# Performance work log

Hardware: AMD Instinct MI355X
Metric: run time of the kernel (lower is better)

Reference implementation:

```python
import jax, jax.numpy as jnp
import numpy as np

B, H, D, E = 64, 8, 64, 512          # batch, heads, head_dim, embed_dim
NB, BS = 32, 128                     # blocks per sequence, block size
L = NB * BS                          # max kv length (4096)
POS = 2048                           # decode position in cache


def setup_inputs() -> dict:
    key = jax.random.key(0)
    ks = jax.random.split(key, 12)
    s = E ** -0.5
    return {
        "hidden_states": jax.random.normal(ks[0], (B, 1, E), jnp.float32),
        "q_w": jax.random.normal(ks[1], (E, E), jnp.float32) * s,
        "q_b": jnp.zeros((E,), jnp.float32),
        "k_w": jax.random.normal(ks[2], (E, E), jnp.float32) * s,
        "k_b": jnp.zeros((E,), jnp.float32),
        "v_w": jax.random.normal(ks[3], (E, E), jnp.float32) * s,
        "v_b": jnp.zeros((E,), jnp.float32),
        "o_w": jax.random.normal(ks[4], (E, E), jnp.float32) * s,
        "o_b": jnp.zeros((E,), jnp.float32),
        "kcache": jax.random.normal(ks[5], (B, H, NB, BS, D), jnp.float32),
        "vcache": jax.random.normal(ks[6], (B, H, NB, BS, D), jnp.float32),
        "attention_mask": jnp.zeros((B, 1, 1, L), jnp.float32),  # additive mask
        "cache_position": POS,
        "block_tables": jax.random.randint(ks[7], (B, NB), 0, NB, jnp.int32),
    }


def reference(hidden_states, q_w, q_b, k_w, k_b, v_w, v_b, o_w, o_b,
              kcache, vcache, attention_mask, cache_position, block_tables):
    scaling = D ** -0.5
    # projections for the single decode token; q is pre-scaled (op gets scale=1.0)
    q = (hidden_states[:, 0] @ q_w.T + q_b).reshape(B, H, D) * scaling
    k_new = (hidden_states[:, 0] @ k_w.T + k_b).reshape(B, H, D)
    v_new = (hidden_states[:, 0] @ v_w.T + v_b).reshape(B, H, D)

    # gather physical blocks per sequence via block table -> [B, NB, H, BS, D]
    bidx = jnp.arange(B)[:, None]
    k_g = kcache[bidx, :, block_tables].transpose(0, 2, 1, 3, 4).reshape(B, H, L, D)
    v_g = vcache[bidx, :, block_tables].transpose(0, 2, 1, 3, 4).reshape(B, H, L, D)

    # write current token's k/v at cache_position (paged cache update)
    k_g = k_g.at[:, :, cache_position, :].set(k_new)
    v_g = v_g.at[:, :, cache_position, :].set(v_new)

    # add-softmax attention: scores = qk + mask
    scores = jnp.einsum('bhd,bhld->bhl', q, k_g) + attention_mask[:, :, 0, :]
    attn = jax.nn.softmax(scores, axis=-1)
    ctx = jnp.einsum('bhl,bhld->bhd', attn, v_g).reshape(B, 1, E)
    return ctx @ o_w.T + o_b
```

## Files before the change

kernel.cpp:

```cpp
#include <hip/hip_runtime.h>
#include <math.h>

#define BB 64
#define HH 8
#define Dh 64
#define EE 512
#define NBLK 32
#define BSZ 128
#define LL 4096
#define BG 4
#define RC 128

typedef float f4 __attribute__((ext_vector_type(4)));

__global__ __launch_bounds__(512) void qkv_proj(
    const float* __restrict__ hidden,
    const float* __restrict__ q_w, const float* __restrict__ q_b,
    const float* __restrict__ k_w, const float* __restrict__ k_b,
    const float* __restrict__ v_w, const float* __restrict__ v_b,
    float* __restrict__ ws)
{
    const int bg = blockIdx.x, proj = blockIdx.y, chunk = blockIdx.z;
    const int tid = threadIdx.x;
    const int r  = tid & (RC - 1);
    const int l4 = tid >> 7;

    __shared__ float sh[BG][EE];
    __shared__ float sp[4][BG][RC];

    for (int i = tid; i < BG * EE; i += 512)
        sh[i >> 9][i & (EE - 1)] = hidden[(bg * BG + (i >> 9)) * EE + (i & (EE - 1))];
    __syncthreads();

    const float* w; const float* bias; float* out; float scale;
    if (proj == 0)      { w = q_w; bias = q_b; out = ws;             scale = 0.125f; }
    else if (proj == 1) { w = k_w; bias = k_b; out = ws + BB * EE;   scale = 1.0f; }
    else                { w = v_w; bias = v_b; out = ws + 2*BB*EE;   scale = 1.0f; }

    const int e = chunk * RC + r;
    const float4* wr = (const float4*)(w + (size_t)e * EE + l4 * 128);
    float acc[BG] = {0.f, 0.f, 0.f, 0.f};
    #pragma unroll 8
    for (int i = 0; i < 32; ++i) {
        const float4 a = wr[i];
        #pragma unroll
        for (int b = 0; b < BG; ++b) {
            const float4 x = ((const float4*)sh[b])[l4 * 32 + i];
            acc[b] += a.x*x.x + a.y*x.y + a.z*x.z + a.w*x.w;
        }
    }
    #pragma unroll
    for (int b = 0; b < BG; ++b) sp[l4][b][r] = acc[b];
    __syncthreads();

    const int b2 = tid >> 7, r2 = tid & (RC - 1);
    const int e2 = chunk * RC + r2;
    const float v = sp[0][b2][r2] + sp[1][b2][r2] + sp[2][b2][r2] + sp[3][b2][r2];
    out[(bg * BG + b2) * EE + e2] = (v + bias[e2]) * scale;
}

__global__ __launch_bounds__(512) void attn(
    const float* __restrict__ ws,
    const float* __restrict__ kcache, const float* __restrict__ vcache,
    const float* __restrict__ mask,
    const int* __restrict__ cpos_p,
    const int* __restrict__ btab,
    float* __restrict__ ctx)
{
    const int bh = blockIdx.x;
    const int b  = bh >> 3;
    const int tid = threadIdx.x;
    const int grp = tid >> 4;
    const int l16 = tid & 15;

    __shared__ float  s_q[Dh];
    __shared__ int    s_bt[NBLK];
    __shared__ float  s_m[32];
    __shared__ float  s_s[32];
    __shared__ float4 s_acc[32][16];

    const float* qv   = ws;
    const float* knew = ws + BB * EE;
    const float* vnew = ws + 2 * BB * EE;

    if (tid < Dh)   s_q[tid]  = qv[(size_t)bh * Dh + tid];
    if (tid < NBLK) s_bt[tid] = btab[b * NBLK + tid];
    const int cpos = *cpos_p;
    __syncthreads();

    const float4 q4 = ((const float4*)s_q)[l16];
    const size_t base = (size_t)bh * NBLK * BSZ * Dh;
    const f4* knew4 = (const f4*)(knew + (size_t)bh * Dh);
    const f4* vnew4 = (const f4*)(vnew + (size_t)bh * Dh);
    const float* mrow = mask + (size_t)b * LL;

    float m = -3.4e38f, s = 0.f;
    float4 acc = make_float4(0.f, 0.f, 0.f, 0.f);

    #pragma unroll 2
    for (int c = 0; c < NBLK; ++c) {
        const size_t pb = base + (size_t)s_bt[c] * (BSZ * Dh);
        #pragma unroll
        for (int s4 = 0; s4 < 4; ++s4) {
            const int rl  = s4 * 32 + grp;
            const int row = c * BSZ + rl;
            const f4* kr = (const f4*)(kcache + pb + (size_t)rl * Dh);
            const f4* vr = (const f4*)(vcache + pb + (size_t)rl * Dh);
            if (row == cpos) { kr = knew4; vr = vnew4; }
            const f4 kv = __builtin_nontemporal_load(kr + l16);
            const f4 vv = __builtin_nontemporal_load(vr + l16);

            float p = q4.x*kv.x + q4.y*kv.y + q4.z*kv.z + q4.w*kv.w;
            p += __shfl_xor(p, 1); p += __shfl_xor(p, 2);
            p += __shfl_xor(p, 4); p += __shfl_xor(p, 8);
            p += mrow[row];

            const float mn = fmaxf(m, p);
            const float cr = __expf(m - mn);
            const float wt = __expf(p - mn);
            s = s * cr + wt;
            acc.x = acc.x * cr + wt * vv.x;
            acc.y = acc.y * cr + wt * vv.y;
            acc.z = acc.z * cr + wt * vv.z;
            acc.w = acc.w * cr + wt * vv.w;
            m = mn;
        }
    }

    if (l16 == 0) { s_m[grp] = m; s_s[grp] = s; }
    s_acc[grp][l16] = acc;
    __syncthreads();

    if (tid < 32) {
        const float mg = s_m[tid];
        float M = mg;
        #pragma unroll
        for (int o = 1; o < 32; o <<= 1) M = fmaxf(M, __shfl_xor(M, o));
        const float c = __expf(mg - M);
        float st = s_s[tid] * c;
        #pragma unroll
        for (int o = 1; o < 32; o <<= 1) st += __shfl_xor(st, o);
        s_m[tid] = c;
        if (tid == 0) s_s[0] = 1.0f / st;
    }
    __syncthreads();

    if (tid < 16) {
        const float inv = s_s[0];
        float4 t = make_float4(0.f, 0.f, 0.f, 0.f);
        #pragma unroll
        for (int g = 0; g < 32; ++g) {
            const float c = s_m[g];
            const float4 u = s_acc[g][tid];
            t.x += c * u.x; t.y += c * u.y; t.z += c * u.z; t.w += c * u.w;
        }
        t.x *= inv; t.y *= inv; t.z *= inv; t.w *= inv;
        ((float4*)(ctx + (size_t)bh * Dh))[tid] = t;
    }
}

__global__ __launch_bounds__(512) void out_proj(
    const float* __restrict__ ctx,
    const float* __restrict__ o_w, const float* __restrict__ o_b,
    float* __restrict__ out)
{
    const int bg = blockIdx.x, chunk = blockIdx.y;
    const int tid = threadIdx.x;
    const int r  = tid & (RC - 1);
    const int l4 = tid >> 7;

    __shared__ float sh[BG][EE];
    __shared__ float sp[4][BG][RC];

    for (int i = tid; i < BG * EE; i += 512)
        sh[i >> 9][i & (EE - 1)] = ctx[(bg * BG + (i >> 9)) * EE + (i & (EE - 1))];
    __syncthreads();

    const int e = chunk * RC + r;
    const float4* wr = (const float4*)(o_w + (size_t)e * EE + l4 * 128);
    float acc[BG] = {0.f, 0.f, 0.f, 0.f};
    #pragma unroll 8
    for (int i = 0; i < 32; ++i) {
        const float4 a = wr[i];
        #pragma unroll
        for (int b = 0; b < BG; ++b) {
            const float4 x = ((const float4*)sh[b])[l4 * 32 + i];
            acc[b] += a.x*x.x + a.y*x.y + a.z*x.z + a.w*x.w;
        }
    }
    #pragma unroll
    for (int b = 0; b < BG; ++b) sp[l4][b][r] = acc[b];
    __syncthreads();

    const int b2 = tid >> 7, r2 = tid & (RC - 1);
    const int e2 = chunk * RC + r2;
    const float v = sp[0][b2][r2] + sp[1][b2][r2] + sp[2][b2][r2] + sp[3][b2][r2];
    out[(bg * BG + b2) * EE + e2] = v + o_b[e2];
}

extern "C" void kernel_launch(void* const* d_in, const int* in_sizes, int n_in,
                              void* d_out, int out_size, void* d_ws, size_t ws_size,
                              hipStream_t stream)
{
    const float* hidden = (const float*)d_in[0];
    const float* q_w = (const float*)d_in[1];
    const float* q_b = (const float*)d_in[2];
    const float* k_w = (const float*)d_in[3];
    const float* k_b = (const float*)d_in[4];
    const float* v_w = (const float*)d_in[5];
    const float* v_b = (const float*)d_in[6];
    const float* o_w = (const float*)d_in[7];
    const float* o_b = (const float*)d_in[8];
    const float* kcache = (const float*)d_in[9];
    const float* vcache = (const float*)d_in[10];
    const float* mask = (const float*)d_in[11];
    const int* cpos = (const int*)d_in[12];
    const int* btab = (const int*)d_in[13];

    float* ws  = (float*)d_ws;
    float* ctx = ws + 3 * BB * EE;

    qkv_proj<<<dim3(BB/BG, 3, EE/RC), 512, 0, stream>>>(hidden, q_w, q_b, k_w, k_b, v_w, v_b, ws);
    attn<<<dim3(BB * HH), 512, 0, stream>>>(ws, kcache, vcache, mask, cpos, btab, ctx);
    out_proj<<<dim3(BB/BG, EE/RC), 512, 0, stream>>>(ctx, o_w, o_b, (float*)d_out);
}
```

Before: 191.1 us.

## Split KV sequence across two partitions per head with separate merge kernel

Splits each (batch, head) attention over the KV blocks into two partitions launched as a 2D grid. Each partition writes an unnormalized partial accumulator plus its running max and sum, and a new merge kernel combines them with log-sum-exp rescaling before the output projection. This doubles the number of blocks to raise memory-level parallelism in the bandwidth-bound attention pass. It adds an extra kernel launch and workspace round-trip.

```diff
diff --git a/kernel.cpp b/kernel.cpp
--- a/kernel.cpp
+++ b/kernel.cpp
@@ -10,8 +10,16 @@
 #define LL 4096
 #define BG 4
 #define RC 128
+#define NPART 2
 
 typedef float f4 __attribute__((ext_vector_type(4)));
+
+#define WS_Q    0
+#define WS_KN   (BB*EE)
+#define WS_VN   (2*BB*EE)
+#define WS_PACC (3*BB*EE)
+#define WS_PMS  (WS_PACC + BB*HH*NPART*Dh)
+#define WS_CTX  (WS_PMS + BB*HH*NPART*2)
 
 __global__ __launch_bounds__(512) void qkv_proj(
     const float* __restrict__ hidden,
@@ -33,9 +41,9 @@
     __syncthreads();
 
     const float* w; const float* bias; float* out; float scale;
-    if (proj == 0)      { w = q_w; bias = q_b; out = ws;             scale = 0.125f; }
-    else if (proj == 1) { w = k_w; bias = k_b; out = ws + BB * EE;   scale = 1.0f; }
-    else                { w = v_w; bias = v_b; out = ws + 2*BB*EE;   scale = 1.0f; }
+    if (proj == 0)      { w = q_w; bias = q_b; out = ws + WS_Q;   scale = 0.125f; }
+    else if (proj == 1) { w = k_w; bias = k_b; out = ws + WS_KN;  scale = 1.0f; }
+    else                { w = v_w; bias = v_b; out = ws + WS_VN;  scale = 1.0f; }
 
     const int e = chunk * RC + r;
     const float4* wr = (const float4*)(w + (size_t)e * EE + l4 * 128);
@@ -65,9 +73,10 @@
     const float* __restrict__ mask,
     const int* __restrict__ cpos_p,
     const int* __restrict__ btab,
-    float* __restrict__ ctx)
-{
-    const int bh = blockIdx.x;
+    float* __restrict__ wsout)
+{
+    const int bh   = blockIdx.x;
+    const int part = blockIdx.y;
     const int b  = bh >> 3;
     const int tid = threadIdx.x;
     const int grp = tid >> 4;
@@ -79,9 +88,9 @@
     __shared__ float  s_s[32];
     __shared__ float4 s_acc[32][16];
 
-    const float* qv   = ws;
-    const float* knew = ws + BB * EE;
-    const float* vnew = ws + 2 * BB * EE;
+    const float* qv   = ws + WS_Q;
+    const float* knew = ws + WS_KN;
+    const float* vnew = ws + WS_VN;
 
     if (tid < Dh)   s_q[tid]  = qv[(size_t)bh * Dh + tid];
     if (tid < NBLK) s_bt[tid] = btab[b * NBLK + tid];
@@ -97,8 +106,10 @@
     float m = -3.4e38f, s = 0.f;
     float4 acc = make_float4(0.f, 0.f, 0.f, 0.f);
 
+    const int c0 = part * (NBLK / NPART);
     #pragma unroll 2
-    for (int c = 0; c < NBLK; ++c) {
+    for (int ci = 0; ci < NBLK / NPART; ++ci) {
+        const int c = c0 + ci;
         const size_t pb = base + (size_t)s_bt[c] * (BSZ * Dh);
         #pragma unroll
         for (int s4 = 0; s4 < 4; ++s4) {
@@ -141,12 +152,12 @@
         #pragma unroll
         for (int o = 1; o < 32; o <<= 1) st += __shfl_xor(st, o);
         s_m[tid] = c;
-        if (tid == 0) s_s[0] = 1.0f / st;
-    }
-    __syncthreads();
-
+        if (tid == 0) { s_s[0] = st; s_s[1] = M; }
+    }
+    __syncthreads();
+
+    const int pidx = bh * NPART + part;
     if (tid < 16) {
-        const float inv = s_s[0];
         float4 t = make_float4(0.f, 0.f, 0.f, 0.f);
         #pragma unroll
         for (int g = 0; g < 32; ++g) {
@@ -154,13 +165,36 @@
             const float4 u = s_acc[g][tid];
             t.x += c * u.x; t.y += c * u.y; t.z += c * u.z; t.w += c * u.w;
         }
-        t.x *= inv; t.y *= inv; t.z *= inv; t.w *= inv;
-        ((float4*)(ctx + (size_t)bh * Dh))[tid] = t;
-    }
+        ((float4*)(wsout + WS_PACC + (size_t)pidx * Dh))[tid] = t;
+        if (tid == 0) {
+            wsout[WS_PMS + pidx * 2 + 0] = s_s[1];
+            wsout[WS_PMS + pidx * 2 + 1] = s_s[0];
+        }
+    }
+}
+
+__global__ __launch_bounds__(512) void merge_parts(
+    const float* __restrict__ ws, float* __restrict__ wsout)
+{
+    const int b = blockIdx.x, t = threadIdx.x;
+    const int h = t >> 6, d = t & 63;
+    const int bh = b * HH + h;
+
+    const float m0 = ws[WS_PMS + (bh * NPART + 0) * 2 + 0];
+    const float s0 = ws[WS_PMS + (bh * NPART + 0) * 2 + 1];
+    const float m1 = ws[WS_PMS + (bh * NPART + 1) * 2 + 0];
+    const float s1 = ws[WS_PMS + (bh * NPART + 1) * 2 + 1];
+    const float M  = fmaxf(m0, m1);
+    const float c0 = __expf(m0 - M), c1 = __expf(m1 - M);
+    const float inv = 1.0f / (c0 * s0 + c1 * s1);
+
+    const float a0 = ws[WS_PACC + (size_t)(bh * NPART + 0) * Dh + d];
+    const float a1 = ws[WS_PACC + (size_t)(bh * NPART + 1) * Dh + d];
+    wsout[WS_CTX + (size_t)bh * Dh + d] = (c0 * a0 + c1 * a1) * inv;
 }
 
 __global__ __launch_bounds__(512) void out_proj(
-    const float* __restrict__ ctx,
+    const float* __restrict__ ws,
     const float* __restrict__ o_w, const float* __restrict__ o_b,
     float* __restrict__ out)
 {
@@ -172,6 +206,7 @@
     __shared__ float sh[BG][EE];
     __shared__ float sp[4][BG][RC];
 
+    const float* ctx = ws + WS_CTX;
     for (int i = tid; i < BG * EE; i += 512)
         sh[i >> 9][i & (EE - 1)] = ctx[(bg * BG + (i >> 9)) * EE + (i & (EE - 1))];
     __syncthreads();
@@ -217,10 +252,10 @@
     const int* cpos = (const int*)d_in[12];
     const int* btab = (const int*)d_in[13];
 
-    float* ws  = (float*)d_ws;
-    float* ctx = ws + 3 * BB * EE;
+    float* ws = (float*)d_ws;
 
     qkv_proj<<<dim3(BB/BG, 3, EE/RC), 512, 0, stream>>>(hidden, q_w, q_b, k_w, k_b, v_w, v_b, ws);
-    attn<<<dim3(BB * HH), 512, 0, stream>>>(ws, kcache, vcache, mask, cpos, btab, ctx);
-    out_proj<<<dim3(BB/BG, EE/RC), 512, 0, stream>>>(ctx, o_w, o_b, (float*)d_out);
-}
+    attn<<<dim3(BB * HH, NPART), 512, 0, stream>>>(ws, kcache, vcache, mask, cpos, btab, ws);
+    merge_parts<<<dim3(BB), 512, 0, stream>>>(ws, ws);
+    out_proj<<<dim3(BB/BG, EE/RC), 512, 0, stream>>>(ws, o_w, o_b, (float*)d_out);
+}
```

Result: slower. 220.6 us (+15.5%).
